# Kernel optimization log

Hardware: AMD Instinct MI355X
Metric: run time of the kernel (lower is better)

## Reference

```python
import jax, jax.numpy as jnp
import numpy as np

H = 1024          # hidden_size
NH = 16           # num_attention_heads
HD = H // NH      # head_dim = 64
FF = 4096         # intermediate_size
EPS = 1e-12       # layer_norm_eps
CLAMP = 1e9


def _layer_norm(x, gamma, beta):
    mu = jnp.mean(x, axis=-1, keepdims=True)
    var = jnp.mean(jnp.square(x - mu), axis=-1, keepdims=True)
    return (x - mu) * jax.lax.rsqrt(var + EPS) * gamma + beta


def setup_inputs() -> dict:
    key = jax.random.key(0)
    ks = jax.random.split(key, 12)
    B, S = 4, 2048
    s_h = 1.0 / np.sqrt(H)
    s_f = 1.0 / np.sqrt(FF)
    return {
        "hidden_states": jax.random.normal(ks[0], (B, S, H), jnp.float32),
        "Wq": jax.random.normal(ks[1], (H, H), jnp.float32) * s_h,
        "bq": jnp.zeros((H,), jnp.float32),
        "Wk": jax.random.normal(ks[2], (H, H), jnp.float32) * s_h,
        "bk": jnp.zeros((H,), jnp.float32),
        "Wv": jax.random.normal(ks[3], (H, H), jnp.float32) * s_h,
        "bv": jnp.zeros((H,), jnp.float32),
        "ln1_g": jnp.ones((H,), jnp.float32),
        "ln1_b": jnp.zeros((H,), jnp.float32),
        "W1": jax.random.normal(ks[4], (H, FF), jnp.float32) * s_h,
        "b1": jnp.zeros((FF,), jnp.float32),
        "W2": jax.random.normal(ks[5], (FF, H), jnp.float32) * s_f,
        "b2": jnp.zeros((H,), jnp.float32),
        "ln2_g": jnp.ones((H,), jnp.float32),
        "ln2_b": jnp.zeros((H,), jnp.float32),
    }


def reference(hidden_states, Wq, bq, Wk, bk, Wv, bv, ln1_g, ln1_b,
              W1, b1, W2, b2, ln2_g, ln2_b):
    B, S, _ = hidden_states.shape
    # QKV projections -> [B, NH, S, HD]
    def heads(x):
        return x.reshape(B, S, NH, HD).transpose(0, 2, 1, 3)
    q = heads(hidden_states @ Wq + bq)
    k = heads(hidden_states @ Wk + bk)
    v = heads(hidden_states @ Wv + bv)
    # manual attention: scale, clamp, softmax + 1e-9 epsilon
    scores = jnp.einsum('bhqd,bhkd->bhqk', q, k) / np.sqrt(HD)
    scores = jnp.clip(scores, -CLAMP, CLAMP)
    probs = jax.nn.softmax(scores, axis=-1) + 1e-9
    ctx = jnp.einsum('bhqk,bhkd->bhqd', probs, v)
    ctx = ctx.transpose(0, 2, 1, 3).reshape(B, S, NH * HD)
    # residual + LN (no output projection in this module)
    x = _layer_norm(hidden_states + ctx, ln1_g, ln1_b)
    # FFN with exact gelu + clamp
    inter = jax.nn.gelu(x @ W1 + b1, approximate=False)
    inter = jnp.clip(inter, -CLAMP, CLAMP)
    out = inter @ W2 + b2
    return _layer_norm(out + x, ln2_g, ln2_b)
```

## Files before the change

kernel.cpp:

```cpp
#include <hip/hip_runtime.h>
#include <math.h>


#define H_   1024
#define NH_  16
#define HD_  64
#define FF_  4096
#define S_   2048
#define B_   4
#define BS_  (B_ * S_)

#define EPI_NONE 0
#define EPI_GELU 1
#define EPI_QKV3 2

typedef unsigned short ushort_t;
typedef short v8s __attribute__((ext_vector_type(8)));
typedef float v4f __attribute__((ext_vector_type(4)));

__device__ __forceinline__ unsigned short f2bf(float f) {
    union { float f; unsigned int u; } v; v.f = f;
    unsigned int u = v.u;
    return (unsigned short)((u + 0x7fffu + ((u >> 16) & 1u)) >> 16);
}
__device__ __forceinline__ unsigned short f2bf_rn(float f) {
    union { float f; unsigned int u; } v; v.f = f;
    return (unsigned short)((v.u + 0x8000u) >> 16);
}
__device__ __forceinline__ float bf2f(unsigned short h) {
    union { unsigned int u; float f; } v; v.u = ((unsigned int)h) << 16;
    return v.f;
}

typedef __attribute__((address_space(1))) void gvoid;
typedef __attribute__((address_space(3))) void lvoid;
__device__ __forceinline__ void async16(const void* g, void* l) {
    __builtin_amdgcn_global_load_lds((gvoid*)g, (lvoid*)l, 16, 0, 0);
}

__global__ __launch_bounds__(256)
void cast_bf16_kernel(const float* __restrict__ x, ushort_t* __restrict__ y)
{
    const size_t i = ((size_t)blockIdx.x * 256 + threadIdx.x) * 4;
    float4 v = *(const float4*)&x[i];
    ushort4 o;
    o.x = f2bf(v.x); o.y = f2bf(v.y); o.z = f2bf(v.z); o.w = f2bf(v.w);
    *(ushort4*)&y[i] = o;
}

__global__ __launch_bounds__(256)
void cast_transpose_kernel(const float* __restrict__ W, ushort_t* __restrict__ Wt,
                           int K, int N)
{
    __shared__ float tile[32][33];
    const int tid = threadIdx.x;
    const int n0 = blockIdx.x * 32, k0 = blockIdx.y * 32;
    const int r  = tid >> 3;
    const int c4 = (tid & 7) * 4;
    float4 v = *(const float4*)&W[(size_t)(k0 + r) * N + n0 + c4];
    tile[r][c4 + 0] = v.x; tile[r][c4 + 1] = v.y;
    tile[r][c4 + 2] = v.z; tile[r][c4 + 3] = v.w;
    __syncthreads();
    ushort4 o;
    o.x = f2bf(tile[c4 + 0][r]); o.y = f2bf(tile[c4 + 1][r]);
    o.z = f2bf(tile[c4 + 2][r]); o.w = f2bf(tile[c4 + 3][r]);
    *(ushort4*)&Wt[(size_t)(n0 + r) * K + k0 + c4] = o;
}

__global__ __launch_bounds__(256)
void concat3_kernel(const float* __restrict__ a, const float* __restrict__ b,
                    const float* __restrict__ c, float* __restrict__ o)
{
    const int i = blockIdx.x * 256 + threadIdx.x;
    o[i] = (i < 1024) ? a[i] : (i < 2048) ? b[i - 1024] : c[i - 2048];
}

template <int EPI>
__global__ __launch_bounds__(256)
void bgemm_kernel(const ushort_t* __restrict__ A, const ushort_t* __restrict__ Bt,
                  const float* __restrict__ bias, void* __restrict__ Cout,
                  int M, int N, int K)
{
    __shared__ ushort_t Atile[128 * 32];
    __shared__ ushort_t Btile[128 * 32];

    const int tid  = threadIdx.x;
    const int wave = tid >> 6;
    const int lane = tid & 63;
    const int ml   = lane & 15;
    const int q8   = lane >> 4;
    const int wm   = wave >> 1, wn = wave & 1;
    const int blockM = blockIdx.y * 128;
    const int blockN = blockIdx.x * 128;

    v4f acc[4][4];
#pragma unroll
    for (int a = 0; a < 4; ++a)
#pragma unroll
        for (int b = 0; b < 4; ++b) acc[a][b] = (v4f)0.f;

    for (int kt = 0; kt < K; kt += 32) {
#pragma unroll
        for (int i = 0; i < 2; ++i) {
            const int chunk = (i * 4 + wave) * 64 + lane;
            const int row = chunk >> 2;
            const int kp  = chunk & 3;
            async16(A  + (size_t)(blockM + row) * K + kt + kp * 8, &Atile[chunk * 8]);
            async16(Bt + (size_t)(blockN + row) * K + kt + kp * 8, &Btile[chunk * 8]);
        }
        __syncthreads();

        v8s af[4], bfr[4];
#pragma unroll
        for (int a = 0; a < 4; ++a)
            af[a] = *(const v8s*)&Atile[(wm * 64 + a * 16 + ml) * 32 + q8 * 8];
#pragma unroll
        for (int b = 0; b < 4; ++b)
            bfr[b] = *(const v8s*)&Btile[(wn * 64 + b * 16 + ml) * 32 + q8 * 8];
#pragma unroll
        for (int a = 0; a < 4; ++a)
#pragma unroll
            for (int b = 0; b < 4; ++b)
                acc[a][b] = __builtin_amdgcn_mfma_f32_16x16x32_bf16(
                    af[a], bfr[b], acc[a][b], 0, 0, 0);
        __syncthreads();
    }

#pragma unroll
    for (int a = 0; a < 4; ++a) {
#pragma unroll
        for (int b = 0; b < 4; ++b) {
            const int n  = blockN + wn * 64 + b * 16 + ml;
            const float bn = bias[n];
            if (EPI == EPI_QKV3) {
                const int nn = n & 1023;
                const int hh = nn >> 6, dd = nn & 63;
                ushort_t* base = (ushort_t*)Cout + (size_t)(n >> 10) * ((size_t)BS_ * H_);
                if (n < 2048) {
#pragma unroll
                    for (int r = 0; r < 4; ++r) {
                        const int m = blockM + wm * 64 + a * 16 + q8 * 4 + r;
                        base[(((size_t)((m >> 11) * NH_ + hh)) * S_ + (m & 2047)) * HD_ + dd]
                            = f2bf(acc[a][b][r] + bn);
                    }
                } else {
                    const int m0 = blockM + wm * 64 + a * 16 + q8 * 4;
                    ushort4 pk;
                    pk.x = f2bf(acc[a][b][0] + bn);
                    pk.y = f2bf(acc[a][b][1] + bn);
                    pk.z = f2bf(acc[a][b][2] + bn);
                    pk.w = f2bf(acc[a][b][3] + bn);
                    *(ushort4*)&base[(((size_t)((m0 >> 11) * NH_ + hh)) * HD_ + dd) * S_
                                     + (m0 & 2047)] = pk;
                }
            } else {
#pragma unroll
                for (int r = 0; r < 4; ++r) {
                    const int m = blockM + wm * 64 + a * 16 + q8 * 4 + r;
                    float v = acc[a][b][r] + bn;
                    if (EPI == EPI_GELU) {
                        v = v * 0.5f * (1.f + erff(v * 0.70710678118654752f));
                        v = fminf(fmaxf(v, -1e9f), 1e9f);
                        ((ushort_t*)Cout)[(size_t)m * N + n] = f2bf(v);
                    } else {
                        ((float*)Cout)[(size_t)m * N + n] = v;
                    }
                }
            }
        }
    }
}

__global__ __launch_bounds__(256)
void vsum_kernel(const ushort_t* __restrict__ VT, float* __restrict__ vsum)
{
    const int bh   = blockIdx.x;
    const int tid  = threadIdx.x;
    const int d    = tid >> 2;
    const int part = tid & 3;
    const ushort_t* p = VT + (size_t)bh * HD_ * S_ + (size_t)d * S_ + part * 512;
    float acc = 0.f;
    for (int i = 0; i < 512; i += 4) {
        ushort4 u = *(const ushort4*)&p[i];
        acc += (bf2f(u.x) + bf2f(u.y)) + (bf2f(u.z) + bf2f(u.w));
    }
    acc += __shfl_xor(acc, 1);
    acc += __shfl_xor(acc, 2);
    if (part == 0) vsum[bh * HD_ + d] = acc;
}

__global__ __launch_bounds__(256)
void flash_kernel(const ushort_t* __restrict__ Q, const ushort_t* __restrict__ Kg,
                  const ushort_t* __restrict__ VT, const float* __restrict__ vsum,
                  float* __restrict__ ctx)
{
    __shared__ ushort_t Qs[64 * 64];
    __shared__ ushort_t Ks[64 * 64];
    __shared__ ushort_t Vs[64 * 64];
    __shared__ ushort_t Pt[64 * 72];

    const int bh   = blockIdx.y;
    const int q0   = blockIdx.x * 64;
    const int tid  = threadIdx.x;
    const int wave = tid >> 6;
    const int lane = tid & 63;
    const int ml   = lane & 15;
    const int q8   = lane >> 4;
    const int sw   = ml & 7;

    const ushort_t* Qp = Q  + (size_t)bh * S_ * HD_ + (size_t)q0 * HD_;
    const ushort_t* Kp = Kg + (size_t)bh * S_ * HD_;
    const ushort_t* Vp = VT + (size_t)bh * HD_ * S_;

#pragma unroll
    for (int i = 0; i < 2; ++i) {
        const int chunk = i * 256 + tid;
        const int row = chunk >> 3, c = chunk & 7;
        async16(Qp + (size_t)row * HD_ + ((c ^ (row & 7)) * 8), &Qs[chunk * 8]);
    }

    const float C_ = 0.18033688011112042f;
    float l_r = 0.f;
    v4f o[4];
#pragma unroll
    for (int g = 0; g < 4; ++g) o[g] = (v4f)0.f;
    v8s qf0, qf1;

    const int prow = (wave * 16 + ml) * 72;

    for (int t = 0; t < S_ / 64; ++t) {
        const int kv0 = t * 64;
        __syncthreads();
#pragma unroll
        for (int i = 0; i < 2; ++i) {
            const int chunk = i * 256 + tid;
            const int row = chunk >> 3, c = chunk & 7;
            async16(Kp + (size_t)(kv0 + row) * HD_ + ((c ^ (row & 7)) * 8),
                    &Ks[chunk * 8]);
        }
#pragma unroll
        for (int i = 0; i < 2; ++i) {
            const int chunk = i * 256 + tid;
            const int row = chunk >> 3, c = chunk & 7;
            async16(Vp + (size_t)row * S_ + kv0 + ((c ^ (row & 7)) * 8),
                    &Vs[chunk * 8]);
        }
        __syncthreads();

        if (t == 0) {
            const int qrow = wave * 16 + ml;
            qf0 = *(const v8s*)&Qs[qrow * 64 + ((q8 ^ sw) * 8)];
            qf1 = *(const v8s*)&Qs[qrow * 64 + (((q8 + 4) ^ sw) * 8)];
        }

#pragma unroll
        for (int a = 0; a < 4; ++a) {
            const int krow = (a * 16 + ml) * 64;
            v8s kf0 = *(const v8s*)&Ks[krow + ((q8 ^ sw) * 8)];
            v8s kf1 = *(const v8s*)&Ks[krow + (((q8 + 4) ^ sw) * 8)];
            v4f z = (v4f)0.f;
            z = __builtin_amdgcn_mfma_f32_16x16x32_bf16(kf0, qf0, z, 0, 0, 0);
            z = __builtin_amdgcn_mfma_f32_16x16x32_bf16(kf1, qf1, z, 0, 0, 0);
            const float p0 = __builtin_exp2f(z[0] * C_);
            const float p1 = __builtin_exp2f(z[1] * C_);
            const float p2 = __builtin_exp2f(z[2] * C_);
            const float p3 = __builtin_exp2f(z[3] * C_);
            l_r += (p0 + p1) + (p2 + p3);
            ushort4 pk;
            pk.x = f2bf_rn(p0); pk.y = f2bf_rn(p1);
            pk.z = f2bf_rn(p2); pk.w = f2bf_rn(p3);
            *(ushort4*)&Pt[prow + a * 16 + q8 * 4] = pk;
        }

        v8s pf0 = *(const v8s*)&Pt[prow + q8 * 8];
        v8s pf1 = *(const v8s*)&Pt[prow + 32 + q8 * 8];
#pragma unroll
        for (int g = 0; g < 4; ++g) {
            const int vrow = (g * 16 + ml) * 64;
            v8s vf0 = *(const v8s*)&Vs[vrow + ((q8 ^ sw) * 8)];
            v8s vf1 = *(const v8s*)&Vs[vrow + (((q8 + 4) ^ sw) * 8)];
            o[g] = __builtin_amdgcn_mfma_f32_16x16x32_bf16(vf0, pf0, o[g], 0, 0, 0);
            o[g] = __builtin_amdgcn_mfma_f32_16x16x32_bf16(vf1, pf1, o[g], 0, 0, 0);
        }
    }

    l_r += __shfl_xor(l_r, 16);
    l_r += __shfl_xor(l_r, 32);

    const int bb = bh >> 4, hh = bh & 15;
    const float linv = 1.f / l_r;
    const int srow = q0 + wave * 16 + ml;
    float* cp = ctx + ((size_t)(bb * S_ + srow)) * H_ + hh * HD_;
#pragma unroll
    for (int g = 0; g < 4; ++g) {
        float4 vs4 = *(const float4*)&vsum[bh * HD_ + g * 16 + q8 * 4];
        float4 ov;
        ov.x = o[g][0] * linv + 1e-9f * vs4.x;
        ov.y = o[g][1] * linv + 1e-9f * vs4.y;
        ov.z = o[g][2] * linv + 1e-9f * vs4.z;
        ov.w = o[g][3] * linv + 1e-9f * vs4.w;
        *(float4*)&cp[g * 16 + q8 * 4] = ov;
    }
}

template <bool WB>
__global__ __launch_bounds__(256)
void add_ln_kernel(const float* __restrict__ A, const float* __restrict__ Bv,
                   const float* __restrict__ gamma, const float* __restrict__ beta,
                   float* __restrict__ out, ushort_t* __restrict__ outb)
{
    const int row = blockIdx.x;
    const int tid = threadIdx.x;
    const float* a = A  + (size_t)row * H_;
    const float* b = Bv + (size_t)row * H_;

    float4 av = *(const float4*)&a[tid * 4];
    float4 bv = *(const float4*)&b[tid * 4];
    float x[4] = { av.x + bv.x, av.y + bv.y, av.z + bv.z, av.w + bv.w };

    float s  = x[0] + x[1] + x[2] + x[3];
    float s2 = x[0]*x[0] + x[1]*x[1] + x[2]*x[2] + x[3]*x[3];
#pragma unroll
    for (int off = 1; off < 64; off <<= 1) {
        s  += __shfl_xor(s,  off);
        s2 += __shfl_xor(s2, off);
    }
    __shared__ float rs[8];
    const int wave = tid >> 6, lane = tid & 63;
    if (lane == 0) { rs[wave] = s; rs[4 + wave] = s2; }
    __syncthreads();
    const float sum  = rs[0] + rs[1] + rs[2] + rs[3];
    const float sum2 = rs[4] + rs[5] + rs[6] + rs[7];
    const float mu   = sum * (1.f / H_);
    const float var  = sum2 * (1.f / H_) - mu * mu;
    const float rstd = rsqrtf(var + 1e-12f);

    float4 gv = *(const float4*)&gamma[tid * 4];
    float4 be = *(const float4*)&beta[tid * 4];
    float4 ov;
    ov.x = (x[0] - mu) * rstd * gv.x + be.x;
    ov.y = (x[1] - mu) * rstd * gv.y + be.y;
    ov.z = (x[2] - mu) * rstd * gv.z + be.z;
    ov.w = (x[3] - mu) * rstd * gv.w + be.w;
    *(float4*)&out[(size_t)row * H_ + tid * 4] = ov;
    if (WB) {
        ushort4 ob;
        ob.x = f2bf(ov.x); ob.y = f2bf(ov.y); ob.z = f2bf(ov.z); ob.w = f2bf(ov.w);
        *(ushort4*)&outb[(size_t)row * H_ + tid * 4] = ob;
    }
}

extern "C" void kernel_launch(void* const* d_in, const int* in_sizes, int n_in,
                              void* d_out, int out_size, void* d_ws, size_t ws_size,
                              hipStream_t stream)
{
    const float* hidden = (const float*)d_in[0];
    const float* Wq     = (const float*)d_in[1];
    const float* bq     = (const float*)d_in[2];
    const float* Wk     = (const float*)d_in[3];
    const float* bk     = (const float*)d_in[4];
    const float* Wv     = (const float*)d_in[5];
    const float* bv     = (const float*)d_in[6];
    const float* ln1_g  = (const float*)d_in[7];
    const float* ln1_b  = (const float*)d_in[8];
    const float* W1     = (const float*)d_in[9];
    const float* b1     = (const float*)d_in[10];
    const float* W2     = (const float*)d_in[11];
    const float* b2     = (const float*)d_in[12];
    const float* ln2_g  = (const float*)d_in[13];
    const float* ln2_b  = (const float*)d_in[14];

    char* ws = (char*)d_ws;
    const size_t MB = 1024 * 1024;
    ushort_t* Xb    = (ushort_t*)(ws + 0);
    ushort_t* x1b   = (ushort_t*)(ws + 0);
    ushort_t* Wqt   = (ushort_t*)(ws + 16 * MB);
    ushort_t* Wkt   = (ushort_t*)(ws + 18 * MB);
    ushort_t* Wvt   = (ushort_t*)(ws + 20 * MB);
    ushort_t* W1t   = (ushort_t*)(ws + 16 * MB);
    ushort_t* W2t   = (ushort_t*)(ws + 24 * MB);
    ushort_t* q     = (ushort_t*)(ws + 32 * MB);
    ushort_t* k     = (ushort_t*)(ws + 48 * MB);
    ushort_t* vt    = (ushort_t*)(ws + 64 * MB);
    float*    ctx   = (float*)(ws + 80 * MB);
    ushort_t* inter = (ushort_t*)(ws + 32 * MB);
    float*    bcat  = (float*)(ws + 96 * MB);
    float*    vsum  = (float*)(ws + 96 * MB + 16384);
    float*    out2  = (float*)(ws + 96 * MB);
    float*    x1    = (float*)(ws + 128 * MB);
    float*    out   = (float*)d_out;

    const dim3 blk(256);

    cast_bf16_kernel<<<dim3(BS_ * H_ / 1024), blk, 0, stream>>>(hidden, Xb);
    cast_transpose_kernel<<<dim3(32, 32),  blk, 0, stream>>>(Wq, Wqt, H_, H_);
    cast_transpose_kernel<<<dim3(32, 32),  blk, 0, stream>>>(Wk, Wkt, H_, H_);
    cast_transpose_kernel<<<dim3(32, 32),  blk, 0, stream>>>(Wv, Wvt, H_, H_);
    cast_transpose_kernel<<<dim3(32, 128), blk, 0, stream>>>(W2, W2t, FF_, H_);
    concat3_kernel<<<dim3(12), blk, 0, stream>>>(bq, bk, bv, bcat);

    bgemm_kernel<EPI_QKV3><<<dim3(24, 64), blk, 0, stream>>>(
        Xb, Wqt, bcat, q, BS_, 3 * H_, H_);

    cast_transpose_kernel<<<dim3(128, 32), blk, 0, stream>>>(W1, W1t, H_, FF_);

    vsum_kernel<<<dim3(B_ * NH_), blk, 0, stream>>>(vt, vsum);

    flash_kernel<<<dim3(S_ / 64, B_ * NH_), blk, 0, stream>>>(q, k, vt, vsum, ctx);

    add_ln_kernel<true><<<dim3(BS_), blk, 0, stream>>>(hidden, ctx, ln1_g, ln1_b, x1, x1b);

    bgemm_kernel<EPI_GELU><<<dim3(32, 64), blk, 0, stream>>>(x1b, W1t, b1, inter, BS_, FF_, H_);

    bgemm_kernel<EPI_NONE><<<dim3(8, 64), blk, 0, stream>>>(inter, W2t, b2, out2, BS_, H_, FF_);

    add_ln_kernel<false><<<dim3(BS_), blk, 0, stream>>>(out2, x1, ln2_g, ln2_b, out, nullptr);
}
```

Measured before the change: 624.9 us.

## Rewrite flash attention with 32x32 MFMA and register-resident probabilities

New measurement: 604.1 us. -3.3%, faster.

```diff
diff --git a/kernel.cpp b/kernel.cpp
--- a/kernel.cpp
+++ b/kernel.cpp
@@ -17,19 +17,27 @@
 typedef unsigned short ushort_t;
 typedef short v8s __attribute__((ext_vector_type(8)));
 typedef float v4f __attribute__((ext_vector_type(4)));
+typedef float v16f __attribute__((ext_vector_type(16)));
+
+#define CQ_ 0.18033688011112042f
 
 __device__ __forceinline__ unsigned short f2bf(float f) {
     union { float f; unsigned int u; } v; v.f = f;
     unsigned int u = v.u;
     return (unsigned short)((u + 0x7fffu + ((u >> 16) & 1u)) >> 16);
 }
-__device__ __forceinline__ unsigned short f2bf_rn(float f) {
-    union { float f; unsigned int u; } v; v.f = f;
-    return (unsigned short)((v.u + 0x8000u) >> 16);
-}
 __device__ __forceinline__ float bf2f(unsigned short h) {
     union { unsigned int u; float f; } v; v.u = ((unsigned int)h) << 16;
     return v.f;
+}
+
+__device__ __forceinline__ unsigned cvt_pk_bf16(float lo, float hi) {
+    unsigned r;
+    asm("v_cvt_pk_bf16_f32 %0, %1, %2" : "=v"(r) : "v"(lo), "v"(hi));
+    return r;
+}
+__device__ __forceinline__ void pl32_swap(unsigned &a, unsigned &b) {
+    asm("v_permlane32_swap_b32 %0, %1" : "+v"(a), "+v"(b));
 }
 
 typedef __attribute__((address_space(1))) void gvoid;
@@ -137,11 +145,12 @@
                 const int hh = nn >> 6, dd = nn & 63;
                 ushort_t* base = (ushort_t*)Cout + (size_t)(n >> 10) * ((size_t)BS_ * H_);
                 if (n < 2048) {
+                    const float sc = (n < 1024) ? CQ_ : 1.f;
 #pragma unroll
                     for (int r = 0; r < 4; ++r) {
                         const int m = blockM + wm * 64 + a * 16 + q8 * 4 + r;
                         base[(((size_t)((m >> 11) * NH_ + hh)) * S_ + (m & 2047)) * HD_ + dd]
-                            = f2bf(acc[a][b][r] + bn);
+                            = f2bf((acc[a][b][r] + bn) * sc);
                     }
                 } else {
                     const int m0 = blockM + wm * 64 + a * 16 + q8 * 4;
@@ -189,117 +198,123 @@
     if (part == 0) vsum[bh * HD_ + d] = acc;
 }
 
-__global__ __launch_bounds__(256)
+__global__ __launch_bounds__(256, 4)
 void flash_kernel(const ushort_t* __restrict__ Q, const ushort_t* __restrict__ Kg,
                   const ushort_t* __restrict__ VT, const float* __restrict__ vsum,
                   float* __restrict__ ctx)
 {
-    __shared__ ushort_t Qs[64 * 64];
+    __shared__ ushort_t Qs[128 * 64];
     __shared__ ushort_t Ks[64 * 64];
     __shared__ ushort_t Vs[64 * 64];
-    __shared__ ushort_t Pt[64 * 72];
-
-    const int bh   = blockIdx.y;
-    const int q0   = blockIdx.x * 64;
+
+    int wg = blockIdx.x;
+    wg = (wg & 7) * 128 + (wg >> 3);
+    const int bh = wg >> 4;
+    const int q0 = (wg & 15) * 128;
+
     const int tid  = threadIdx.x;
     const int wave = tid >> 6;
     const int lane = tid & 63;
-    const int ml   = lane & 15;
-    const int q8   = lane >> 4;
-    const int sw   = ml & 7;
+    const int m    = lane & 31;
+    const int hi   = lane >> 5;
 
     const ushort_t* Qp = Q  + (size_t)bh * S_ * HD_ + (size_t)q0 * HD_;
     const ushort_t* Kp = Kg + (size_t)bh * S_ * HD_;
     const ushort_t* Vp = VT + (size_t)bh * HD_ * S_;
 
 #pragma unroll
-    for (int i = 0; i < 2; ++i) {
-        const int chunk = i * 256 + tid;
-        const int row = chunk >> 3, c = chunk & 7;
-        async16(Qp + (size_t)row * HD_ + ((c ^ (row & 7)) * 8), &Qs[chunk * 8]);
-    }
-
-    const float C_ = 0.18033688011112042f;
-    float l_r = 0.f;
-    v4f o[4];
-#pragma unroll
-    for (int g = 0; g < 4; ++g) o[g] = (v4f)0.f;
-    v8s qf0, qf1;
-
-    const int prow = (wave * 16 + ml) * 72;
+    for (int i = 0; i < 4; ++i) {
+        const int ch = i * 256 + tid;
+        const int row = ch >> 3, c = ch & 7;
+        async16(Qp + (size_t)row * HD_ + ((c ^ (row & 7)) * 8), &Qs[ch * 8]);
+    }
+
+    v16f o0 = (v16f)0.f, o1 = (v16f)0.f;
+    float lp0 = 0.f, lp1 = 0.f, lp2 = 0.f, lp3 = 0.f;
+    v8s qf[4];
+    v8s pf[4];
 
     for (int t = 0; t < S_ / 64; ++t) {
         const int kv0 = t * 64;
         __syncthreads();
 #pragma unroll
         for (int i = 0; i < 2; ++i) {
-            const int chunk = i * 256 + tid;
-            const int row = chunk >> 3, c = chunk & 7;
+            const int ch = i * 256 + tid;
+            const int row = ch >> 3, c = ch & 7;
             async16(Kp + (size_t)(kv0 + row) * HD_ + ((c ^ (row & 7)) * 8),
-                    &Ks[chunk * 8]);
-        }
-#pragma unroll
-        for (int i = 0; i < 2; ++i) {
-            const int chunk = i * 256 + tid;
-            const int row = chunk >> 3, c = chunk & 7;
+                    &Ks[ch * 8]);
             async16(Vp + (size_t)row * S_ + kv0 + ((c ^ (row & 7)) * 8),
-                    &Vs[chunk * 8]);
+                    &Vs[ch * 8]);
         }
         __syncthreads();
 
         if (t == 0) {
-            const int qrow = wave * 16 + ml;
-            qf0 = *(const v8s*)&Qs[qrow * 64 + ((q8 ^ sw) * 8)];
-            qf1 = *(const v8s*)&Qs[qrow * 64 + (((q8 + 4) ^ sw) * 8)];
-        }
-
-#pragma unroll
-        for (int a = 0; a < 4; ++a) {
-            const int krow = (a * 16 + ml) * 64;
-            v8s kf0 = *(const v8s*)&Ks[krow + ((q8 ^ sw) * 8)];
-            v8s kf1 = *(const v8s*)&Ks[krow + (((q8 + 4) ^ sw) * 8)];
-            v4f z = (v4f)0.f;
-            z = __builtin_amdgcn_mfma_f32_16x16x32_bf16(kf0, qf0, z, 0, 0, 0);
-            z = __builtin_amdgcn_mfma_f32_16x16x32_bf16(kf1, qf1, z, 0, 0, 0);
-            const float p0 = __builtin_exp2f(z[0] * C_);
-            const float p1 = __builtin_exp2f(z[1] * C_);
-            const float p2 = __builtin_exp2f(z[2] * C_);
-            const float p3 = __builtin_exp2f(z[3] * C_);
-            l_r += (p0 + p1) + (p2 + p3);
-            ushort4 pk;
-            pk.x = f2bf_rn(p0); pk.y = f2bf_rn(p1);
-            pk.z = f2bf_rn(p2); pk.w = f2bf_rn(p3);
-            *(ushort4*)&Pt[prow + a * 16 + q8 * 4] = pk;
-        }
-
-        v8s pf0 = *(const v8s*)&Pt[prow + q8 * 8];
-        v8s pf1 = *(const v8s*)&Pt[prow + 32 + q8 * 8];
-#pragma unroll
-        for (int g = 0; g < 4; ++g) {
-            const int vrow = (g * 16 + ml) * 64;
-            v8s vf0 = *(const v8s*)&Vs[vrow + ((q8 ^ sw) * 8)];
-            v8s vf1 = *(const v8s*)&Vs[vrow + (((q8 + 4) ^ sw) * 8)];
-            o[g] = __builtin_amdgcn_mfma_f32_16x16x32_bf16(vf0, pf0, o[g], 0, 0, 0);
-            o[g] = __builtin_amdgcn_mfma_f32_16x16x32_bf16(vf1, pf1, o[g], 0, 0, 0);
-        }
-    }
-
-    l_r += __shfl_xor(l_r, 16);
+            const int qrow = wave * 32 + m;
+#pragma unroll
+            for (int c = 0; c < 4; ++c)
+                qf[c] = *(const v8s*)&Qs[qrow * 64 + (((2 * c + hi) ^ (qrow & 7)) * 8)];
+        }
+
+#pragma unroll
+        for (int a = 0; a < 2; ++a) {
+            v16f z = (v16f)0.f;
+            const int krow = a * 32 + m;
+#pragma unroll
+            for (int c = 0; c < 4; ++c) {
+                v8s kf = *(const v8s*)&Ks[krow * 64 + (((2 * c + hi) ^ (m & 7)) * 8)];
+                z = __builtin_amdgcn_mfma_f32_32x32x16_bf16(kf, qf[c], z, 0, 0, 0);
+            }
+            unsigned u[8];
+#pragma unroll
+            for (int mm = 0; mm < 8; ++mm) {
+                const float plo = __builtin_exp2f(z[2 * mm]);
+                const float phi = __builtin_exp2f(z[2 * mm + 1]);
+                if ((mm & 3) == 0)      lp0 += plo + phi;
+                else if ((mm & 3) == 1) lp1 += plo + phi;
+                else if ((mm & 3) == 2) lp2 += plo + phi;
+                else                    lp3 += plo + phi;
+                u[mm] = cvt_pk_bf16(plo, phi);
+            }
+            pl32_swap(u[0], u[2]); pl32_swap(u[1], u[3]);
+            pl32_swap(u[4], u[6]); pl32_swap(u[5], u[7]);
+            union { unsigned w[4]; v8s s; } c0, c1;
+            c0.w[0] = u[0]; c0.w[1] = u[1]; c0.w[2] = u[2]; c0.w[3] = u[3];
+            c1.w[0] = u[4]; c1.w[1] = u[5]; c1.w[2] = u[6]; c1.w[3] = u[7];
+            pf[2 * a]     = c0.s;
+            pf[2 * a + 1] = c1.s;
+        }
+
+#pragma unroll
+        for (int c = 0; c < 4; ++c) {
+            const int sw = ((2 * c + hi) ^ (m & 7)) * 8;
+            v8s vf0 = *(const v8s*)&Vs[m * 64 + sw];
+            v8s vf1 = *(const v8s*)&Vs[(32 + m) * 64 + sw];
+            o0 = __builtin_amdgcn_mfma_f32_32x32x16_bf16(vf0, pf[c], o0, 0, 0, 0);
+            o1 = __builtin_amdgcn_mfma_f32_32x32x16_bf16(vf1, pf[c], o1, 0, 0, 0);
+        }
+    }
+
+    float l_r = (lp0 + lp1) + (lp2 + lp3);
     l_r += __shfl_xor(l_r, 32);
+    const float linv = 1.f / l_r;
 
     const int bb = bh >> 4, hh = bh & 15;
-    const float linv = 1.f / l_r;
-    const int srow = q0 + wave * 16 + ml;
+    const int srow = q0 + wave * 32 + m;
     float* cp = ctx + ((size_t)(bb * S_ + srow)) * H_ + hh * HD_;
 #pragma unroll
-    for (int g = 0; g < 4; ++g) {
-        float4 vs4 = *(const float4*)&vsum[bh * HD_ + g * 16 + q8 * 4];
-        float4 ov;
-        ov.x = o[g][0] * linv + 1e-9f * vs4.x;
-        ov.y = o[g][1] * linv + 1e-9f * vs4.y;
-        ov.z = o[g][2] * linv + 1e-9f * vs4.z;
-        ov.w = o[g][3] * linv + 1e-9f * vs4.w;
-        *(float4*)&cp[g * 16 + q8 * 4] = ov;
+    for (int g = 0; g < 2; ++g) {
+        const v16f& o = g ? o1 : o0;
+#pragma unroll
+        for (int rq = 0; rq < 4; ++rq) {
+            const int d0 = g * 32 + rq * 8 + hi * 4;
+            float4 vs4 = *(const float4*)&vsum[bh * HD_ + d0];
+            float4 ov;
+            ov.x = o[rq * 4 + 0] * linv + 1e-9f * vs4.x;
+            ov.y = o[rq * 4 + 1] * linv + 1e-9f * vs4.y;
+            ov.z = o[rq * 4 + 2] * linv + 1e-9f * vs4.z;
+            ov.w = o[rq * 4 + 3] * linv + 1e-9f * vs4.w;
+            *(float4*)&cp[d0] = ov;
+        }
     }
 }
 
@@ -406,7 +421,7 @@
 
     vsum_kernel<<<dim3(B_ * NH_), blk, 0, stream>>>(vt, vsum);
 
-    flash_kernel<<<dim3(S_ / 64, B_ * NH_), blk, 0, stream>>>(q, k, vt, vsum, ctx);
+    flash_kernel<<<dim3((S_ / 128) * (B_ * NH_)), blk, 0, stream>>>(q, k, vt, vsum, ctx);
 
     add_ln_kernel<true><<<dim3(BS_), blk, 0, stream>>>(hidden, ctx, ln1_g, ln1_b, x1, x1b);
 
```
